# Performance work log

Hardware: AMD Instinct MI355X
Metric: run time of the kernel (lower is better)

Reference implementation:

```python
import jax, jax.numpy as jnp
import numpy as np

NEG_SLOPE = 0.2

def gat_conv(x, edge, W, att_src, att_dst, bias, heads, out_ch, concat):
    # x: [N, F_in], edge: [2, E] (self-loops already included)
    N = x.shape[0]
    src, dst = edge[0], edge[1]
    h = (x @ W).reshape(N, heads, out_ch)                     # [N, H, C]
    a_src = jnp.sum(h * att_src, axis=-1)                     # [N, H]
    a_dst = jnp.sum(h * att_dst, axis=-1)                     # [N, H]
    e = jax.nn.leaky_relu(a_src[src] + a_dst[dst], NEG_SLOPE)  # [E, H]
    # segment softmax over incoming edges of each dst node
    e_max = jax.ops.segment_max(e, dst, num_segments=N)       # [N, H]
    e_exp = jnp.exp(e - e_max[dst])                           # [E, H]
    denom = jax.ops.segment_sum(e_exp, dst, num_segments=N)   # [N, H]
    alpha = e_exp / denom[dst]                                # [E, H]
    msg = h[src] * alpha[:, :, None]                          # [E, H, C]
    out = jax.ops.segment_sum(msg, dst, num_segments=N)       # [N, H, C]
    if concat:
        out = out.reshape(N, heads * out_ch)
    else:
        out = out.mean(axis=1)
    return out + bias


def setup_inputs() -> dict:
    key = jax.random.key(0)
    ks = jax.random.split(key, 10)
    N, E = 50000, 1600000
    F_in, H, C1, n_cls = 256, 4, 64, 40
    x = jax.random.normal(ks[0], (N, F_in), dtype=jnp.float32)
    edge_index = jax.random.randint(ks[1], (2, E), 0, N, dtype=jnp.int64)
    s1 = 1.0 / np.sqrt(F_in)
    s2 = 1.0 / np.sqrt(H * C1)
    return {
        "x": x,
        "edge_index": edge_index,
        "W1": jax.random.normal(ks[2], (F_in, H * C1), dtype=jnp.float32) * s1,
        "att_src1": jax.random.normal(ks[3], (H, C1), dtype=jnp.float32) * s2,
        "att_dst1": jax.random.normal(ks[4], (H, C1), dtype=jnp.float32) * s2,
        "b1": jnp.zeros((H * C1,), dtype=jnp.float32),
        "W2": jax.random.normal(ks[5], (H * C1, n_cls), dtype=jnp.float32) * s2,
        "att_src2": jax.random.normal(ks[6], (1, n_cls), dtype=jnp.float32) * 0.1,
        "att_dst2": jax.random.normal(ks[7], (1, n_cls), dtype=jnp.float32) * 0.1,
        "b2": jnp.zeros((n_cls,), dtype=jnp.float32),
    }


def reference(x, edge_index, W1, att_src1, att_dst1, b1, W2, att_src2, att_dst2, b2):
    N = x.shape[0]
    # PyG GATConv adds self-loops by default
    loops = jnp.arange(N, dtype=edge_index.dtype)
    edge = jnp.concatenate([edge_index, jnp.stack([loops, loops])], axis=1)
    # dropout is identity in eval mode
    h = gat_conv(x, edge, W1, att_src1, att_dst1, b1, heads=4, out_ch=64, concat=True)
    h = jax.nn.elu(h)
    out = gat_conv(h, edge, W2, att_src2, att_dst2, b2, heads=1, out_ch=40, concat=False)
    return out
```

## Files before the change

kernel.cpp:

```cpp
#include <hip/hip_runtime.h>
#include <hip/hip_bf16.h>

typedef short bf16x8 __attribute__((ext_vector_type(8)));
typedef float f32x4 __attribute__((ext_vector_type(4)));
typedef float f32x2 __attribute__((ext_vector_type(2)));
typedef unsigned short u16x8 __attribute__((ext_vector_type(8)));

#define CHUNK 4096
#define BCAP 16384

__device__ __forceinline__ float wred_sum(float v) {
  #pragma unroll
  for (int off = 32; off > 0; off >>= 1)
    v += __shfl_xor(v, off, 64);
  return v;
}
__device__ __forceinline__ float b2f(unsigned short u) {
  union { unsigned int i; float f; } x;
  x.i = ((unsigned int)u) << 16;
  return x.f;
}
__device__ __forceinline__ unsigned short f2bu(float f) {
  __hip_bfloat16 b = __float2bfloat16(f);
  return *(unsigned short*)&b;
}
__device__ __forceinline__ void pkfma(f32x2& acc, f32x2 v, f32x2 w) {
  asm("v_pk_fma_f32 %0, %1, %2, %0" : "+v"(acc) : "v"(v), "v"(w));
}
__device__ __forceinline__ void qfma(f32x2* acc2, unsigned int u, f32x2 wp) {
  f32x2 a, b;
  a[0] = (float)(u & 0xFFu);         a[1] = (float)((u >> 8) & 0xFFu);
  b[0] = (float)((u >> 16) & 0xFFu); b[1] = (float)(u >> 24);
  pkfma(acc2[0], a, wp);
  pkfma(acc2[1], b, wp);
}
__device__ __forceinline__ void bffma(f32x2& acc, unsigned int up, f32x2 wp) {
  union { unsigned int i; float f; } lo, hi;
  lo.i = up << 16; hi.i = up & 0xFFFF0000u;
  f32x2 v; v[0] = lo.f; v[1] = hi.f;
  pkfma(acc, v, wp);
}
__device__ __forceinline__ float ldf(const void* p, long long i, int is16) {
  return is16 ? __bfloat162float(((const __hip_bfloat16*)p)[i])
              : ((const float*)p)[i];
}
__device__ __forceinline__ int edge_at(const int* e, long long idx, int is64) {
  return is64 ? (int)((const long long*)e)[idx] : e[idx];
}

__global__ void detect_kernel(const int* __restrict__ edge, int n_edge_check,
                              const unsigned int* __restrict__ xw, int n_x_check,
                              int* __restrict__ flag,
                              int* __restrict__ bcursor, int NB) {
  __shared__ int s_nz, s_cnt, s_tot;
  int tid = threadIdx.x;
  for (int b = tid; b < NB; b += 256) bcursor[b] = b * BCAP;
  if (tid == 0) { s_nz = 0; s_cnt = 0; s_tot = 0; }
  __syncthreads();
  int nz = 0;
  for (int k = tid; k < n_edge_check; k += 256)
    if (edge[2 * k + 1] != 0) nz = 1;
  if (nz) atomicOr(&s_nz, 1);
  int c = 0, t = 0;
  for (int k = tid; k < n_x_check; k += 256) {
    unsigned int w = xw[k];
    if (w == 0u) continue;
    t++;
    unsigned int e = (w >> 7) & 0xFFu;
    if (e >= 100u && e <= 150u) c++;
  }
  atomicAdd(&s_cnt, c);
  atomicAdd(&s_tot, t);
  __syncthreads();
  if (tid == 0) {
    flag[0] = (s_nz == 0) ? 1 : 0;
    flag[1] = (s_cnt * 10 > s_tot * 6) ? 1 : 0;
  }
}

__global__ __launch_bounds__(256) void part_prep_kernel(
    const int* __restrict__ edge, int E, int N, const int* __restrict__ flag,
    int* __restrict__ bcursor, unsigned int* __restrict__ part, int NB, int nch,
    const void* __restrict__ W1v, const void* __restrict__ W2v,
    __hip_bfloat16* __restrict__ Wt1, __hip_bfloat16* __restrict__ Wt2,
    int F, int HC, int C2, int C2p) {
  __shared__ int cnt[1024];
  __shared__ int loff[1025];
  __shared__ int gpos[1024];
  __shared__ int lcur[1024];
  __shared__ unsigned int staged[CHUNK];
  __shared__ int staged_addr[CHUNK];
  __shared__ int s[256];
  __shared__ int rbase;
  int tid = threadIdx.x;
  int f16 = flag[1];
  if (blockIdx.x >= nch) {
    long long i = (long long)(blockIdx.x - nch) * 256 + tid;
    int n1 = HC * F;
    if (i < n1) {
      int idx = (int)i;
      int n = idx / F, k = idx - n * F;
      Wt1[idx] = __float2bfloat16(ldf(W1v, (long long)k * HC + n, f16));
    } else {
      int jj = (int)(i - n1);
      if (jj >= C2p * HC) return;
      int n = jj / HC, k = jj - n * HC;
      float v = (n < C2) ? ldf(W2v, (long long)k * C2 + n, f16) : 0.f;
      Wt2[jj] = __float2bfloat16(v);
    }
    return;
  }
  long long base = (long long)blockIdx.x * CHUNK;
  long long total = (long long)E + N;
  int maxa = NB * BCAP - 1;
  int here = (int)min((long long)CHUNK, total - base);
  for (int b = tid; b < NB; b += 256) cnt[b] = 0;
  if (tid == 0) rbase = 0;
  __syncthreads();
  int is64 = flag[0];
  int myb[16];
  unsigned int myp[16];
  #pragma unroll
  for (int j = 0; j < 16; j++) {
    long long i = base + j * 256 + tid;
    myb[j] = -1;
    if (i < total) {
      int d, sv;
      if (i < E) {
        sv = edge_at(edge, i, is64);
        d = edge_at(edge, (long long)E + i, is64);
      } else {
        sv = d = (int)(i - E);
      }
      d = min(max(d, 0), N - 1);
      sv = min(max(sv, 0), N - 1);
      myb[j] = d >> 8;
      myp[j] = ((unsigned int)(d & 255) << 24) | (unsigned int)sv;
      atomicAdd(&cnt[myb[j]], 1);
    }
  }
  __syncthreads();
  for (int c0 = 0; c0 < NB; c0 += 256) {
    int idx = c0 + tid;
    int v = (idx < NB) ? cnt[idx] : 0;
    s[tid] = v;
    __syncthreads();
    for (int off = 1; off < 256; off <<= 1) {
      int t = (tid >= off) ? s[tid - off] : 0;
      __syncthreads();
      s[tid] += t;
      __syncthreads();
    }
    int mb = rbase;
    if (idx < NB) loff[idx] = mb + s[tid] - v;
    __syncthreads();
    if (tid == 0) rbase = mb + s[255];
    __syncthreads();
  }
  __syncthreads();
  for (int b = tid; b < NB; b += 256) {
    int c = cnt[b];
    gpos[b] = c ? atomicAdd(&bcursor[b], c) : 0;
    lcur[b] = loff[b];
  }
  __syncthreads();
  #pragma unroll
  for (int j = 0; j < 16; j++) {
    if (myb[j] >= 0) {
      int b = myb[j];
      int slot = atomicAdd(&lcur[b], 1);
      staged[slot] = myp[j];
      staged_addr[slot] = min(gpos[b] + (slot - loff[b]), maxa);
    }
  }
  __syncthreads();
  for (int i = tid; i < here; i += 256)
    part[staged_addr[i]] = staged[i];
}

__global__ __launch_bounds__(256) void bsort_gemm_kernel(
    const unsigned int* __restrict__ part, const int* __restrict__ bcursor,
    int N, int* __restrict__ indptr, int* __restrict__ iend,
    int* __restrict__ ssrc, int NBS,
    const void* __restrict__ A, const __hip_bfloat16* __restrict__ BtT,
    const void* __restrict__ attS, const void* __restrict__ attD,
    float* __restrict__ aD, float2* __restrict__ aSq, int NT,
    int M, int K,
    unsigned char* __restrict__ h1q,
    const int* __restrict__ dflag) {
  __shared__ int hist[256], cur[256];
  __shared__ int s[256];
  int tid = threadIdx.x;
  if (blockIdx.x < NBS) {
    int b = blockIdx.x;
    int begin = b * BCAP, end = bcursor[b];
    hist[tid] = 0;
    __syncthreads();
    for (int i = begin + tid; i < end; i += 256)
      atomicAdd(&hist[part[i] >> 24], 1);
    __syncthreads();
    int v = hist[tid];
    s[tid] = v;
    __syncthreads();
    for (int off = 1; off < 256; off <<= 1) {
      int t = (tid >= off) ? s[tid - off] : 0;
      __syncthreads();
      s[tid] += t;
      __syncthreads();
    }
    int exc = s[tid] - v;
    cur[tid] = exc;
    int d = b * 256 + tid;
    if (d < N) { indptr[d] = begin + exc; iend[d] = begin + exc + v; }
    __syncthreads();
    for (int i = begin + tid; i < end; i += 256) {
      unsigned int p = part[i];
      int pos = begin + atomicAdd(&cur[p >> 24], 1);
      ssrc[pos] = (int)(p & 0xFFFFFFu);
    }
    return;
  }
  int nwg = gridDim.x - NBS;
  int i0 = blockIdx.x - NBS;
  int qd = nwg >> 3, rm = nwg & 7;
  int xcd = i0 & 7, idx = i0 >> 3;
  int logical = (xcd < rm ? xcd * (qd + 1) : rm * (qd + 1) + (xcd - rm) * qd) + idx;
  int colt = logical % NT;
  int rowt = logical / NT;
  int row0 = rowt * 64, col0 = colt * 64;

  int f16 = dflag[1];
  int w = tid >> 6, l = tid & 63;
  int m_lane = l & 15, q = l >> 4;
  int arow = row0 + w * 16 + m_lane;
  bool aok = (arow < M);
  const __hip_bfloat16* Ab = (const __hip_bfloat16*)A + (long long)arow * K + q * 8;
  const float* Af = (const float*)A + (long long)arow * K + q * 8;
  const __hip_bfloat16* Brow = BtT + (long long)(col0 + m_lane) * K + q * 8;
  f32x4 acc[4] = {};
  #pragma unroll 4
  for (int k0 = 0; k0 < K; k0 += 32) {
    bf16x8 af = {};
    if (aok) {
      if (f16) {
        af = *(const bf16x8*)(Ab + k0);
      } else {
        float4 u0 = *(const float4*)(Af + k0);
        float4 u1 = *(const float4*)(Af + k0 + 4);
        af[0] = (short)f2bu(u0.x); af[1] = (short)f2bu(u0.y);
        af[2] = (short)f2bu(u0.z); af[3] = (short)f2bu(u0.w);
        af[4] = (short)f2bu(u1.x); af[5] = (short)f2bu(u1.y);
        af[6] = (short)f2bu(u1.z); af[7] = (short)f2bu(u1.w);
      }
    }
    #pragma unroll
    for (int t = 0; t < 4; t++) {
      bf16x8 bf = *(const bf16x8*)(Brow + (long long)t * 16 * K + k0);
      acc[t] = __builtin_amdgcn_mfma_f32_16x16x32_bf16(af, bf, acc[t], 0, 0, 0);
    }
  }
  #pragma unroll
  for (int r = 0; r < 4; r++) {
    int gr = row0 + w * 16 + q * 4 + r;
    float ps = 0.f, pd = 0.f, vmax = 0.f;
    #pragma unroll
    for (int t = 0; t < 4; t++) {
      float v = acc[t][r];
      int gc = col0 + t * 16 + m_lane;
      ps += v * ldf(attS, gc, f16);
      pd += v * ldf(attD, gc, f16);
      vmax = fmaxf(vmax, fabsf(v));
    }
    #pragma unroll
    for (int off = 1; off < 16; off <<= 1) {
      ps += __shfl_xor(ps, off, 64);
      pd += __shfl_xor(pd, off, 64);
      vmax = fmaxf(vmax, __shfl_xor(vmax, off, 64));
    }
    if (gr < M) {
      float qinv = (vmax > 0.f) ? 127.f / vmax : 0.f;
      #pragma unroll
      for (int t = 0; t < 4; t++) {
        int gc = col0 + t * 16 + m_lane;
        h1q[(long long)gr * 256 + gc] =
            (unsigned char)(__float2int_rn(acc[t][r] * qinv) + 128);
      }
      if (m_lane == 0) {
        float2 sq; sq.x = ps; sq.y = vmax * (1.f / 127.f);
        aSq[(long long)gr * NT + colt] = sq;
        aD[(long long)gr * NT + colt] = pd;
      }
    }
  }
}

__global__ __launch_bounds__(256) void mfma_gemm_kernel(
    const void* __restrict__ A, const __hip_bfloat16* __restrict__ BtT,
    __hip_bfloat16* __restrict__ Cb,
    const void* __restrict__ attS, const void* __restrict__ attD,
    float* __restrict__ aS, float* __restrict__ aD, int NT,
    int M, int Nout, int K,
    const int* __restrict__ dflag) {
  int nwg = gridDim.x;
  int i0 = blockIdx.x;
  int qd = nwg >> 3, rm = nwg & 7;
  int xcd = i0 & 7, idx = i0 >> 3;
  int logical = (xcd < rm ? xcd * (qd + 1) : rm * (qd + 1) + (xcd - rm) * qd) + idx;
  int colt = logical % NT;
  int rowt = logical / NT;
  int row0 = rowt * 64, col0 = colt * 64;

  int f16 = dflag[1];
  int tid = threadIdx.x;
  int w = tid >> 6, l = tid & 63;
  int m_lane = l & 15, q = l >> 4;
  int arow = row0 + w * 16 + m_lane;
  bool aok = (arow < M);
  const __hip_bfloat16* Ab = (const __hip_bfloat16*)A + (long long)arow * K + q * 8;
  const __hip_bfloat16* Brow = BtT + (long long)(col0 + m_lane) * K + q * 8;
  f32x4 acc[4] = {};
  #pragma unroll 4
  for (int k0 = 0; k0 < K; k0 += 32) {
    bf16x8 af = {};
    if (aok) af = *(const bf16x8*)(Ab + k0);
    #pragma unroll
    for (int t = 0; t < 4; t++) {
      bf16x8 bf = *(const bf16x8*)(Brow + (long long)t * 16 * K + k0);
      acc[t] = __builtin_amdgcn_mfma_f32_16x16x32_bf16(af, bf, acc[t], 0, 0, 0);
    }
  }
  #pragma unroll
  for (int r = 0; r < 4; r++) {
    int gr = row0 + w * 16 + q * 4 + r;
    float ps = 0.f, pd = 0.f;
    #pragma unroll
    for (int t = 0; t < 4; t++) {
      int gc = col0 + t * 16 + m_lane;
      float v = acc[t][r];
      if (gc < Nout) {
        ps += v * ldf(attS, gc, f16);
        pd += v * ldf(attD, gc, f16);
        if (gr < M) Cb[(long long)gr * Nout + gc] = __float2bfloat16(v);
      }
    }
    #pragma unroll
    for (int off = 1; off < 16; off <<= 1) {
      ps += __shfl_xor(ps, off, 64);
      pd += __shfl_xor(pd, off, 64);
    }
    if (m_lane == 0 && gr < M) {
      aS[(long long)gr * NT + colt] = ps;
      aD[(long long)gr * NT + colt] = pd;
    }
  }
}

__global__ __launch_bounds__(256) void aggregate1_kernel(
    const int* __restrict__ indptr, const int* __restrict__ iend,
    const int* __restrict__ ssrc,
    const unsigned char* __restrict__ h1q, const float2* __restrict__ a_sq,
    const float* __restrict__ a_dst, const void* __restrict__ b1,
    __hip_bfloat16* __restrict__ h2b, int N, const int* __restrict__ dflag) {
  int f16 = dflag[1];
  int w = threadIdx.x >> 6, l = threadIdx.x & 63;
  int d = blockIdx.x * 4 + w;
  if (d >= N) return;
  int q = l >> 4;
  int e16 = l & 15;
  int hb = (l & 12) << 2;
  int chb = (l & 15) << 4;
  int begin = indptr[d], end = iend[d];
  float adst = a_dst[d * 4 + q];
  int s0 = ssrc[begin];
  float den = 0.f, accS = 0.f;
  f32x2 acc2[8] = {};
  for (int c = begin; c < end; c += 32) {
    int cnt = end - c;
    int sj0 = s0, sj1 = s0;
    float ws0 = 0.f, ws1 = 0.f;
    if (e16 < cnt) {
      sj0 = ssrc[c + e16];
      float2 t = a_sq[sj0 * 4 + q];
      float e = t.x + adst;
      e = (e > 0.f) ? e : 0.2f * e;
      float wj = __expf(e);
      den += wj; ws0 = wj * t.y;
    }
    if (e16 + 16 < cnt) {
      sj1 = ssrc[c + 16 + e16];
      float2 t = a_sq[sj1 * 4 + q];
      float e = t.x + adst;
      e = (e > 0.f) ? e : 0.2f * e;
      float wj = __expf(e);
      den += wj; ws1 = wj * t.y;
    }
    int m0 = cnt < 16 ? cnt : 16;
    int m1 = cnt - 16; m1 = m1 < 0 ? 0 : (m1 > 16 ? 16 : m1);
    int j0 = (m0 + 3) >> 2, j1 = (m1 + 3) >> 2;
    #pragma unroll 4
    for (int j = 0; j < j0; j++) {
      int idx = hb + 4 * j + q;
      int s = __shfl(sj0, idx, 64);
      float wt = __shfl(ws0, idx, 64);
      accS += wt;
      f32x2 wp; wp[0] = wt; wp[1] = wt;
      uint4 uv = *(const uint4*)(h1q + (long long)s * 256 + chb);
      qfma(&acc2[0], uv.x, wp);
      qfma(&acc2[2], uv.y, wp);
      qfma(&acc2[4], uv.z, wp);
      qfma(&acc2[6], uv.w, wp);
    }
    #pragma unroll 4
    for (int j = 0; j < j1; j++) {
      int idx = hb + 4 * j + q;
      int s = __shfl(sj1, idx, 64);
      float wt = __shfl(ws1, idx, 64);
      accS += wt;
      f32x2 wp; wp[0] = wt; wp[1] = wt;
      uint4 uv = *(const uint4*)(h1q + (long long)s * 256 + chb);
      qfma(&acc2[0], uv.x, wp);
      qfma(&acc2[2], uv.y, wp);
      qfma(&acc2[4], uv.z, wp);
      qfma(&acc2[6], uv.w, wp);
    }
  }
  float* af = (float*)acc2;
  #pragma unroll
  for (int i = 0; i < 16; i++) {
    af[i] += __shfl_xor(af[i], 16, 64);
    af[i] += __shfl_xor(af[i], 32, 64);
  }
  accS += __shfl_xor(accS, 16, 64);
  accS += __shfl_xor(accS, 32, 64);
  #pragma unroll
  for (int off = 1; off < 16; off <<= 1)
    den += __shfl_xor(den, off, 64);
  float deh = __shfl(den, hb, 64);
  float inv = 1.f / deh;
  if (l < 16) {
    u16x8 o0, o1;
    #pragma unroll
    for (int i = 0; i < 16; i++) {
      float v = (af[i] - 128.f * accS) * inv + ldf(b1, chb + i, f16);
      v = (v > 0.f) ? v : (__expf(v) - 1.f);
      if (i < 8) o0[i] = f2bu(v); else o1[i - 8] = f2bu(v);
    }
    u16x8* dst = (u16x8*)((unsigned short*)h2b + (long long)d * 256 + chb);
    dst[0] = o0;
    dst[1] = o1;
  }
}

__global__ __launch_bounds__(256) void aggregate2_kernel(
    const int* __restrict__ indptr, const int* __restrict__ iend,
    const int* __restrict__ ssrc,
    const __hip_bfloat16* __restrict__ gb, const float* __restrict__ a_src,
    const float* __restrict__ a_dst, const void* __restrict__ b2,
    void* __restrict__ out, int N, int C, const int* __restrict__ dflag) {
  int f16 = dflag[1];
  int w = threadIdx.x >> 6, l = threadIdx.x & 63;
  int d = blockIdx.x * 4 + w;
  if (d >= N) return;
  int begin = indptr[d], end = iend[d];
  float adst = a_dst[d];
  int eg = l / 10;
  int cq = l - eg * 10;
  bool act = (eg < 6);
  int s0 = ssrc[begin];
  float den = 0.f;
  f32x2 acc01 = {0.f, 0.f}, acc23 = {0.f, 0.f};
  for (int c = begin; c < end; c += 64) {
    int cnt = min(64, end - c);
    int sj = s0;
    float wj = 0.f;
    if (l < cnt) {
      sj = ssrc[c + l];
      float e = a_src[sj] + adst;
      e = (e > 0.f) ? e : 0.2f * e;
      wj = __expf(e);
    }
    den += wj;
    int jm = (cnt + 5) / 6;
    #pragma unroll 4
    for (int j = 0; j < jm; j++) {
      int idx = 6 * j + eg;
      int s = __shfl(sj, idx & 63, 64);
      float wt = __shfl(wj, idx & 63, 64);
      if (!act || idx >= cnt) wt = 0.f;
      uint2 gv = *(const uint2*)((const unsigned short*)gb +
                                 (long long)s * C + 4 * cq);
      f32x2 wp; wp[0] = wt; wp[1] = wt;
      bffma(acc01, gv.x, wp);
      bffma(acc23, gv.y, wp);
    }
  }
  den = wred_sum(den);
  float inv = 1.f / den;
  float a0 = acc01[0], a1 = acc01[1], a2 = acc23[0], a3 = acc23[1];
  #pragma unroll
  for (int k = 1; k < 6; k++) {
    int srcl = cq + 10 * k;
    a0 += __shfl(acc01[0], srcl, 64);
    a1 += __shfl(acc01[1], srcl, 64);
    a2 += __shfl(acc23[0], srcl, 64);
    a3 += __shfl(acc23[1], srcl, 64);
  }
  if (l < 10) {
    float v0 = a0 * inv + ldf(b2, 4 * l + 0, f16);
    float v1 = a1 * inv + ldf(b2, 4 * l + 1, f16);
    float v2 = a2 * inv + ldf(b2, 4 * l + 2, f16);
    float v3 = a3 * inv + ldf(b2, 4 * l + 3, f16);
    long long o = (long long)d * C + 4 * l;
    if (f16) {
      ushort4 ov;
      ov.x = f2bu(v0); ov.y = f2bu(v1); ov.z = f2bu(v2); ov.w = f2bu(v3);
      *(ushort4*)((unsigned short*)out + o) = ov;
    } else {
      float4 ov;
      ov.x = v0; ov.y = v1; ov.z = v2; ov.w = v3;
      *(float4*)((float*)out + o) = ov;
    }
  }
}

extern "C" void kernel_launch(void* const* d_in, const int* in_sizes, int n_in,
                              void* d_out, int out_size, void* d_ws, size_t ws_size,
                              hipStream_t stream) {
  const void* x   = d_in[0];
  const int* edge = (const int*)d_in[1];
  const void* W1  = d_in[2];
  const void* as1 = d_in[3];
  const void* ad1 = d_in[4];
  const void* b1  = d_in[5];
  const void* W2  = d_in[6];
  const void* as2 = d_in[7];
  const void* ad2 = d_in[8];
  const void* b2  = d_in[9];

  const int F  = 256;
  const int HC = 256;
  const int N  = in_sizes[0] / F;
  const int E  = in_sizes[1] / 2;
  const int C2 = in_sizes[9];
  const int C2p = 64;
  const int total = E + N;
  const int NB = (N + 255) / 256;
  const int Mpad = ((N + 63) / 64) * 64;

  char* p = (char*)d_ws;
  auto alloc = [&](size_t bytes) -> void* {
    void* r = (void*)p;
    p += (bytes + 255) & ~(size_t)255;
    return r;
  };
  unsigned char*  h1q = (unsigned char*)alloc((size_t)Mpad * HC);
  __hip_bfloat16* h2b = (__hip_bfloat16*)alloc((size_t)Mpad * HC * 2);
  __hip_bfloat16* gb  = (__hip_bfloat16*)alloc((size_t)Mpad * C2 * 2);
  __hip_bfloat16* Wt1 = (__hip_bfloat16*)alloc((size_t)HC * F * 2);
  __hip_bfloat16* Wt2 = (__hip_bfloat16*)alloc((size_t)C2p * HC * 2);
  float2* a_sq1 = (float2*)alloc((size_t)N * 4 * 8);
  float* a_dst1 = (float*)alloc((size_t)N * 4 * 4);
  float* a_src2 = (float*)alloc((size_t)N * 4);
  float* a_dst2 = (float*)alloc((size_t)N * 4);
  unsigned int* part = (unsigned int*)alloc((size_t)NB * BCAP * 4);
  int* ssrc     = (int*)alloc((size_t)NB * BCAP * 4);
  int* bcursor  = (int*)alloc((size_t)NB * 4);
  int* indptr   = (int*)alloc((size_t)N * 4);
  int* iend     = (int*)alloc((size_t)N * 4);
  int* flag     = (int*)alloc(256);

  detect_kernel<<<1, 256, 0, stream>>>(edge, E < 2048 ? E : 2048,
                                       (const unsigned int*)x, 4096, flag,
                                       bcursor, NB);

  int nch = (total + CHUNK - 1) / CHUNK;
  int nprep = (HC * F + C2p * HC + 255) / 256;
  part_prep_kernel<<<nch + nprep, 256, 0, stream>>>(
      edge, E, N, flag, bcursor, part, NB, nch,
      W1, W2, Wt1, Wt2, F, HC, C2, C2p);

  bsort_gemm_kernel<<<NB + 4 * (Mpad / 64), 256, 0, stream>>>(
      part, bcursor, N, indptr, iend, ssrc, NB,
      x, Wt1, as1, ad1, a_dst1, a_sq1, 4, N, F, h1q, flag);

  aggregate1_kernel<<<(N + 3) / 4, 256, 0, stream>>>(indptr, iend, ssrc, h1q, a_sq1,
                                                     a_dst1, b1, h2b, N, flag);

  mfma_gemm_kernel<<<Mpad / 64, 256, 0, stream>>>(
      h2b, Wt2, gb, as2, ad2, a_src2, a_dst2, 1,
      N, C2, HC, flag);
  aggregate2_kernel<<<(N + 3) / 4, 256, 0, stream>>>(indptr, iend, ssrc, gb, a_src2, a_dst2,
                                                     b2, d_out, N, C2, flag);
}
```

Measured before the change: 359.5 us.

## Co-schedule edge partitioning with layer-1 GEMM and split bucket sort out

The weight-transpose prep moves to its own small kernel. Edge partitioning now shares a launch with the layer-1 GEMM, so the scatter work overlaps the matrix multiply, and the per-bucket sort becomes a separate kernel after it. Partition chunks shrink to 2048 edges with 256-bucket shared arrays, which cuts LDS use and raises occupancy. In exchange there is one extra launch, the code assumes NB ≤ 256 (N ≤ 65536), and more blocks do global atomics on bcursor.

```diff
diff --git a/kernel.cpp b/kernel.cpp
--- a/kernel.cpp
+++ b/kernel.cpp
@@ -6,7 +6,7 @@
 typedef float f32x2 __attribute__((ext_vector_type(2)));
 typedef unsigned short u16x8 __attribute__((ext_vector_type(8)));
 
-#define CHUNK 4096
+#define CHUNK2 2048
 #define BCAP 16384
 
 __device__ __forceinline__ float wred_sum(float v) {
@@ -78,71 +78,73 @@
   }
 }
 
-__global__ __launch_bounds__(256) void part_prep_kernel(
+__global__ void prep_kernel(const void* __restrict__ W1v, const void* __restrict__ W2v,
+                            __hip_bfloat16* __restrict__ Wt1, __hip_bfloat16* __restrict__ Wt2,
+                            int F, int HC, int C2, int C2p,
+                            const int* __restrict__ dflag) {
+  int f16 = dflag[1];
+  int i = blockIdx.x * 256 + threadIdx.x;
+  int n1 = HC * F;
+  if (i < n1) {
+    int n = i / F, k = i - n * F;
+    Wt1[i] = __float2bfloat16(ldf(W1v, (long long)k * HC + n, f16));
+  } else {
+    int jj = i - n1;
+    if (jj >= C2p * HC) return;
+    int n = jj / HC, k = jj - n * HC;
+    float v = (n < C2) ? ldf(W2v, (long long)k * C2 + n, f16) : 0.f;
+    Wt2[jj] = __float2bfloat16(v);
+  }
+}
+
+__global__ __launch_bounds__(256) void part_gemm_kernel(
     const int* __restrict__ edge, int E, int N, const int* __restrict__ flag,
-    int* __restrict__ bcursor, unsigned int* __restrict__ part, int NB, int nch,
-    const void* __restrict__ W1v, const void* __restrict__ W2v,
-    __hip_bfloat16* __restrict__ Wt1, __hip_bfloat16* __restrict__ Wt2,
-    int F, int HC, int C2, int C2p) {
-  __shared__ int cnt[1024];
-  __shared__ int loff[1025];
-  __shared__ int gpos[1024];
-  __shared__ int lcur[1024];
-  __shared__ unsigned int staged[CHUNK];
-  __shared__ int staged_addr[CHUNK];
+    int* __restrict__ bcursor, unsigned int* __restrict__ part, int NB, int npart,
+    const void* __restrict__ A, const __hip_bfloat16* __restrict__ BtT,
+    const void* __restrict__ attS, const void* __restrict__ attD,
+    float* __restrict__ aD, float2* __restrict__ aSq, int NT,
+    int M, int K,
+    unsigned char* __restrict__ h1q) {
+  __shared__ int cnt[256];
+  __shared__ int loff[256];
+  __shared__ int gpos[256];
+  __shared__ int lcur[256];
+  __shared__ unsigned int staged[CHUNK2];
+  __shared__ int staged_addr[CHUNK2];
   __shared__ int s[256];
-  __shared__ int rbase;
   int tid = threadIdx.x;
   int f16 = flag[1];
-  if (blockIdx.x >= nch) {
-    long long i = (long long)(blockIdx.x - nch) * 256 + tid;
-    int n1 = HC * F;
-    if (i < n1) {
-      int idx = (int)i;
-      int n = idx / F, k = idx - n * F;
-      Wt1[idx] = __float2bfloat16(ldf(W1v, (long long)k * HC + n, f16));
-    } else {
-      int jj = (int)(i - n1);
-      if (jj >= C2p * HC) return;
-      int n = jj / HC, k = jj - n * HC;
-      float v = (n < C2) ? ldf(W2v, (long long)k * C2 + n, f16) : 0.f;
-      Wt2[jj] = __float2bfloat16(v);
-    }
-    return;
-  }
-  long long base = (long long)blockIdx.x * CHUNK;
-  long long total = (long long)E + N;
-  int maxa = NB * BCAP - 1;
-  int here = (int)min((long long)CHUNK, total - base);
-  for (int b = tid; b < NB; b += 256) cnt[b] = 0;
-  if (tid == 0) rbase = 0;
-  __syncthreads();
-  int is64 = flag[0];
-  int myb[16];
-  unsigned int myp[16];
-  #pragma unroll
-  for (int j = 0; j < 16; j++) {
-    long long i = base + j * 256 + tid;
-    myb[j] = -1;
-    if (i < total) {
-      int d, sv;
-      if (i < E) {
-        sv = edge_at(edge, i, is64);
-        d = edge_at(edge, (long long)E + i, is64);
-      } else {
-        sv = d = (int)(i - E);
+  if (blockIdx.x < npart) {
+    long long base = (long long)blockIdx.x * CHUNK2;
+    long long total = (long long)E + N;
+    int maxa = NB * BCAP - 1;
+    int here = (int)min((long long)CHUNK2, total - base);
+    cnt[tid] = 0;
+    __syncthreads();
+    int is64 = flag[0];
+    int myb[8];
+    unsigned int myp[8];
+    #pragma unroll
+    for (int j = 0; j < 8; j++) {
+      long long i = base + j * 256 + tid;
+      myb[j] = -1;
+      if (i < total) {
+        int d, sv;
+        if (i < E) {
+          sv = edge_at(edge, i, is64);
+          d = edge_at(edge, (long long)E + i, is64);
+        } else {
+          sv = d = (int)(i - E);
+        }
+        d = min(max(d, 0), N - 1);
+        sv = min(max(sv, 0), N - 1);
+        myb[j] = d >> 8;
+        myp[j] = ((unsigned int)(d & 255) << 24) | (unsigned int)sv;
+        atomicAdd(&cnt[myb[j]], 1);
       }
-      d = min(max(d, 0), N - 1);
-      sv = min(max(sv, 0), N - 1);
-      myb[j] = d >> 8;
-      myp[j] = ((unsigned int)(d & 255) << 24) | (unsigned int)sv;
-      atomicAdd(&cnt[myb[j]], 1);
-    }
-  }
-  __syncthreads();
-  for (int c0 = 0; c0 < NB; c0 += 256) {
-    int idx = c0 + tid;
-    int v = (idx < NB) ? cnt[idx] : 0;
+    }
+    __syncthreads();
+    int v = cnt[tid];
     s[tid] = v;
     __syncthreads();
     for (int off = 1; off < 256; off <<= 1) {
@@ -151,77 +153,27 @@
       s[tid] += t;
       __syncthreads();
     }
-    int mb = rbase;
-    if (idx < NB) loff[idx] = mb + s[tid] - v;
-    __syncthreads();
-    if (tid == 0) rbase = mb + s[255];
-    __syncthreads();
-  }
-  __syncthreads();
-  for (int b = tid; b < NB; b += 256) {
-    int c = cnt[b];
-    gpos[b] = c ? atomicAdd(&bcursor[b], c) : 0;
-    lcur[b] = loff[b];
-  }
-  __syncthreads();
-  #pragma unroll
-  for (int j = 0; j < 16; j++) {
-    if (myb[j] >= 0) {
-      int b = myb[j];
-      int slot = atomicAdd(&lcur[b], 1);
-      staged[slot] = myp[j];
-      staged_addr[slot] = min(gpos[b] + (slot - loff[b]), maxa);
-    }
-  }
-  __syncthreads();
-  for (int i = tid; i < here; i += 256)
-    part[staged_addr[i]] = staged[i];
-}
-
-__global__ __launch_bounds__(256) void bsort_gemm_kernel(
-    const unsigned int* __restrict__ part, const int* __restrict__ bcursor,
-    int N, int* __restrict__ indptr, int* __restrict__ iend,
-    int* __restrict__ ssrc, int NBS,
-    const void* __restrict__ A, const __hip_bfloat16* __restrict__ BtT,
-    const void* __restrict__ attS, const void* __restrict__ attD,
-    float* __restrict__ aD, float2* __restrict__ aSq, int NT,
-    int M, int K,
-    unsigned char* __restrict__ h1q,
-    const int* __restrict__ dflag) {
-  __shared__ int hist[256], cur[256];
-  __shared__ int s[256];
-  int tid = threadIdx.x;
-  if (blockIdx.x < NBS) {
-    int b = blockIdx.x;
-    int begin = b * BCAP, end = bcursor[b];
-    hist[tid] = 0;
-    __syncthreads();
-    for (int i = begin + tid; i < end; i += 256)
-      atomicAdd(&hist[part[i] >> 24], 1);
-    __syncthreads();
-    int v = hist[tid];
-    s[tid] = v;
-    __syncthreads();
-    for (int off = 1; off < 256; off <<= 1) {
-      int t = (tid >= off) ? s[tid - off] : 0;
-      __syncthreads();
-      s[tid] += t;
-      __syncthreads();
-    }
     int exc = s[tid] - v;
-    cur[tid] = exc;
-    int d = b * 256 + tid;
-    if (d < N) { indptr[d] = begin + exc; iend[d] = begin + exc + v; }
-    __syncthreads();
-    for (int i = begin + tid; i < end; i += 256) {
-      unsigned int p = part[i];
-      int pos = begin + atomicAdd(&cur[p >> 24], 1);
-      ssrc[pos] = (int)(p & 0xFFFFFFu);
-    }
+    loff[tid] = exc;
+    lcur[tid] = exc;
+    gpos[tid] = (tid < NB && v) ? atomicAdd(&bcursor[tid], v) : 0;
+    __syncthreads();
+    #pragma unroll
+    for (int j = 0; j < 8; j++) {
+      if (myb[j] >= 0) {
+        int b = myb[j];
+        int slot = atomicAdd(&lcur[b], 1);
+        staged[slot] = myp[j];
+        staged_addr[slot] = min(gpos[b] + (slot - loff[b]), maxa);
+      }
+    }
+    __syncthreads();
+    for (int i = tid; i < here; i += 256)
+      part[staged_addr[i]] = staged[i];
     return;
   }
-  int nwg = gridDim.x - NBS;
-  int i0 = blockIdx.x - NBS;
+  int nwg = gridDim.x - npart;
+  int i0 = blockIdx.x - npart;
   int qd = nwg >> 3, rm = nwg & 7;
   int xcd = i0 & 7, idx = i0 >> 3;
   int logical = (xcd < rm ? xcd * (qd + 1) : rm * (qd + 1) + (xcd - rm) * qd) + idx;
@@ -229,7 +181,6 @@
   int rowt = logical / NT;
   int row0 = rowt * 64, col0 = colt * 64;
 
-  int f16 = dflag[1];
   int w = tid >> 6, l = tid & 63;
   int m_lane = l & 15, q = l >> 4;
   int arow = row0 + w * 16 + m_lane;
@@ -291,6 +242,41 @@
         aD[(long long)gr * NT + colt] = pd;
       }
     }
+  }
+}
+
+__global__ __launch_bounds__(256) void bucket_sort_kernel(
+    const unsigned int* __restrict__ part, const int* __restrict__ bcursor,
+    int N, int* __restrict__ indptr, int* __restrict__ iend,
+    int* __restrict__ ssrc) {
+  __shared__ int hist[256], cur[256];
+  __shared__ int s[256];
+  int tid = threadIdx.x;
+  int b = blockIdx.x;
+  int begin = b * BCAP, end = bcursor[b];
+  hist[tid] = 0;
+  __syncthreads();
+  for (int i = begin + tid; i < end; i += 256)
+    atomicAdd(&hist[part[i] >> 24], 1);
+  __syncthreads();
+  int v = hist[tid];
+  s[tid] = v;
+  __syncthreads();
+  for (int off = 1; off < 256; off <<= 1) {
+    int t = (tid >= off) ? s[tid - off] : 0;
+    __syncthreads();
+    s[tid] += t;
+    __syncthreads();
+  }
+  int exc = s[tid] - v;
+  cur[tid] = exc;
+  int d = b * 256 + tid;
+  if (d < N) { indptr[d] = begin + exc; iend[d] = begin + exc + v; }
+  __syncthreads();
+  for (int i = begin + tid; i < end; i += 256) {
+    unsigned int p = part[i];
+    int pos = begin + atomicAdd(&cur[p >> 24], 1);
+    ssrc[pos] = (int)(p & 0xFFFFFFu);
   }
 }
 
@@ -573,15 +559,15 @@
                                        (const unsigned int*)x, 4096, flag,
                                        bcursor, NB);
 
-  int nch = (total + CHUNK - 1) / CHUNK;
   int nprep = (HC * F + C2p * HC + 255) / 256;
-  part_prep_kernel<<<nch + nprep, 256, 0, stream>>>(
-      edge, E, N, flag, bcursor, part, NB, nch,
-      W1, W2, Wt1, Wt2, F, HC, C2, C2p);
-
-  bsort_gemm_kernel<<<NB + 4 * (Mpad / 64), 256, 0, stream>>>(
-      part, bcursor, N, indptr, iend, ssrc, NB,
-      x, Wt1, as1, ad1, a_dst1, a_sq1, 4, N, F, h1q, flag);
+  prep_kernel<<<nprep, 256, 0, stream>>>(W1, W2, Wt1, Wt2, F, HC, C2, C2p, flag);
+
+  int npart = (total + CHUNK2 - 1) / CHUNK2;
+  part_gemm_kernel<<<npart + 4 * (Mpad / 64), 256, 0, stream>>>(
+      edge, E, N, flag, bcursor, part, NB, npart,
+      x, Wt1, as1, ad1, a_dst1, a_sq1, 4, N, F, h1q);
+
+  bucket_sort_kernel<<<NB, 256, 0, stream>>>(part, bcursor, N, indptr, iend, ssrc);
 
   aggregate1_kernel<<<(N + 3) / 4, 256, 0, stream>>>(indptr, iend, ssrc, h1q, a_sq1,
                                                      a_dst1, b1, h2b, N, flag);
```

After: 360.4 us. About the same (+0.3%).
